# Kernel tuning notes

Measured on AMD Instinct MI355X. Metric: run time of the kernel, lower is better.

The kernel has to match this reference:

```python
import jax, jax.numpy as jnp
import numpy as np

E = 2          # e_layers
DM = 64        # d_model == emb_dim (hardcoded 64 in out_layer)
H = 8          # n_heads
DH = DM // H
DFF = 256      # d_ff
P = 16         # patch_size
STRIDE = P // 2
SL = 4096      # seq_len
NPATCH = (SL - P) // STRIDE + 1   # 511
PRED = 96
B, M = 8, 8
FACTOR = 5
EPS = 1e-5


def setup_inputs() -> dict:
    key = jax.random.key(0)
    ks = jax.random.split(key, 32)
    s = jnp.float32(0.02)
    f = lambda i, shape: jax.random.normal(ks[i], shape, jnp.float32)
    d = {
        "x_enc": f(0, (B, SL, M)),
        "x_mark_enc": f(1, (B, SL, 4)),
        "x_dec": f(2, (B, PRED, M)),
        "x_mark_dec": f(3, (B, PRED, 4)),
        # patch embedding  Linear(patch_size -> emb_dim)
        "in_W": f(4, (DM, P)) * s,
        "in_b": jnp.zeros((DM,), jnp.float32),
        # per-layer attention projections (stacked over e_layers)
        "Wq": f(5, (E, DM, DM)) * s, "bq": jnp.zeros((E, DM), jnp.float32),
        "Wk": f(6, (E, DM, DM)) * s, "bk": jnp.zeros((E, DM), jnp.float32),
        "Wv": f(7, (E, DM, DM)) * s, "bv": jnp.zeros((E, DM), jnp.float32),
        "Wo": f(8, (E, DM, DM)) * s, "bo": jnp.zeros((E, DM), jnp.float32),
        # FFN (Conv1d kernel=1 == Linear)
        "c1_W": f(9, (E, DFF, DM)) * s, "c1_b": jnp.zeros((E, DFF), jnp.float32),
        "c2_W": f(10, (E, DM, DFF)) * s, "c2_b": jnp.zeros((E, DM), jnp.float32),
        # layer norms
        "ln1_g": jnp.ones((E, DM), jnp.float32), "ln1_b": jnp.zeros((E, DM), jnp.float32),
        "ln2_g": jnp.ones((E, DM), jnp.float32), "ln2_b": jnp.zeros((E, DM), jnp.float32),
        "lnf_g": jnp.ones((DM,), jnp.float32), "lnf_b": jnp.zeros((DM,), jnp.float32),
        # decode head  Linear(64*num_patches -> pred_len)
        "out_W": f(11, (PRED, DM * NPATCH)) * s,
        "out_b": jnp.zeros((PRED,), jnp.float32),
    }
    return d


def _ln(x, g, b):
    mu = x.mean(-1, keepdims=True)
    var = ((x - mu) ** 2).mean(-1, keepdims=True)
    return (x - mu) * jax.lax.rsqrt(var + EPS) * g + b


def _prob_attn(q, k, v, key):
    # q,k,v: [Bn, H, L, Dh]  (ProbSparse attention, mask_flag=False)
    Bn, h, Lq, Dh = q.shape
    Lk = k.shape[2]
    U_part = min(int(FACTOR * np.ceil(np.log(Lk))), Lk)   # sampled keys per query
    u = min(int(FACTOR * np.ceil(np.log(Lq))), Lq)        # top-u active queries
    idx = jax.random.randint(key, (Lq, U_part), 0, Lk)
    k_sample = k[:, :, idx, :]                             # [Bn,H,Lq,U,Dh]
    qk_sample = jnp.einsum('bhld,bhlud->bhlu', q, k_sample)
    # sparsity measure: max - sum/L_K (as in torch code)
    sparsity = qk_sample.max(-1) - qk_sample.sum(-1) / jnp.float32(Lk)
    _, top_idx = jax.lax.top_k(sparsity, u)                # [Bn,H,u]
    q_red = jnp.take_along_axis(q, top_idx[..., None], axis=2)  # [Bn,H,u,Dh]
    scale = jax.lax.rsqrt(jnp.float32(Dh))
    scores = jnp.einsum('bhud,bhkd->bhuk', q_red, k) * scale    # [Bn,H,u,Lk]
    attn = jax.nn.softmax(scores, axis=-1)
    # lazy context: mean of V for inactive queries, attn@V for active ones
    ctx = jnp.broadcast_to(v.mean(axis=2, keepdims=True), q.shape)
    upd = jnp.einsum('bhuk,bhkd->bhud', attn, v)
    bi = jnp.arange(Bn)[:, None, None]
    hi = jnp.arange(h)[None, :, None]
    ctx = ctx.at[bi, hi, top_idx].set(upd)
    return ctx.transpose(0, 2, 1, 3)  # [Bn,L,H,Dh]


def reference(x_enc, x_mark_enc, x_dec, x_mark_dec, in_W, in_b, Wq, bq, Wk, bk,
              Wv, bv, Wo, bo, c1_W, c1_b, c2_W, c2_b, ln1_g, ln1_b, ln2_g, ln2_b,
              lnf_g, lnf_b, out_W, out_b):
    Bb, L, Mm = x_enc.shape
    x = x_enc.transpose(0, 2, 1)  # b l m -> b m l
    pidx = jnp.arange(NPATCH)[:, None] * STRIDE + jnp.arange(P)[None, :]
    patches = x[:, :, pidx]                         # [B,M,N,P] (unfold)
    z = patches.reshape(Bb * Mm, NPATCH, P) @ in_W.T + in_b  # [BM,N,DM]
    akey = jax.random.key(1)
    for e in range(E):
        q = (z @ Wq[e].T + bq[e]).reshape(Bb * Mm, NPATCH, H, DH).transpose(0, 2, 1, 3)
        k = (z @ Wk[e].T + bk[e]).reshape(Bb * Mm, NPATCH, H, DH).transpose(0, 2, 1, 3)
        v = (z @ Wv[e].T + bv[e]).reshape(Bb * Mm, NPATCH, H, DH).transpose(0, 2, 1, 3)
        ctx = _prob_attn(q, k, v, jax.random.fold_in(akey, e))
        new_x = ctx.reshape(Bb * Mm, NPATCH, DM) @ Wo[e].T + bo[e]
        x1 = _ln(z + new_x, ln1_g[e], ln1_b[e])
        y = jax.nn.gelu(x1 @ c1_W[e].T + c1_b[e], approximate=False)
        y = y @ c2_W[e].T + c2_b[e]
        z = _ln(x1 + y, ln2_g[e], ln2_b[e])
    z = _ln(z, lnf_g, lnf_b)
    out = z.reshape(Bb * Mm, -1) @ out_W.T + out_b   # [BM, pred_len]
    out = out.reshape(Bb, Mm, PRED).transpose(0, 2, 1)  # (b m) l -> b l m
    return out[:, -PRED:, :]
```

## Files before the change

kernel.cpp:

```cpp
#include <hip/hip_runtime.h>
#include <hip/hip_bf16.h>
#include <stdint.h>
#include <math.h>

typedef __hip_bfloat16 bf16;
typedef __attribute__((ext_vector_type(8))) short short8;
typedef __attribute__((ext_vector_type(4))) short short4v;
typedef __attribute__((ext_vector_type(4))) float fx4;

#define NP 511
#define UPART 35
#define NTOK 32704
#define NBITS 17885
#define LN_EPS 1e-5f

__host__ __device__ __forceinline__ void tf2x32(uint32_t k0, uint32_t k1,
                                                uint32_t x0, uint32_t x1,
                                                uint32_t* o0, uint32_t* o1) {
  uint32_t ks2 = k0 ^ k1 ^ 0x1BD11BDAu;
  x0 += k0; x1 += k1;
#define TFR(r) { x0 += x1; x1 = (x1 << (r)) | (x1 >> (32 - (r))); x1 ^= x0; }
  TFR(13) TFR(15) TFR(26) TFR(6)   x0 += k1;  x1 += ks2 + 1u;
  TFR(17) TFR(29) TFR(16) TFR(24)  x0 += ks2; x1 += k0 + 2u;
  TFR(13) TFR(15) TFR(26) TFR(6)   x0 += k0;  x1 += k1 + 3u;
  TFR(17) TFR(29) TFR(16) TFR(24)  x0 += k1;  x1 += ks2 + 4u;
  TFR(13) TFR(15) TFR(26) TFR(6)   x0 += ks2; x1 += k0 + 5u;
#undef TFR
  *o0 = x0; *o1 = x1;
}

__device__ __forceinline__ float ldin(const void* p, int i, int f32) {
  if (f32) return ((const float*)p)[i];
  return __bfloat162float(((const bf16*)p)[i]);
}
__device__ __forceinline__ unsigned short f2bf(float v) {
  uint32_t u = __builtin_bit_cast(uint32_t, v);
  u += 0x7fffu + ((u >> 16) & 1u);
  return (unsigned short)(u >> 16);
}
__device__ __forceinline__ float bfb2f(uint32_t h) {
  uint32_t u = h << 16;
  return __builtin_bit_cast(float, u);
}
__device__ __forceinline__ float lo16(uint32_t w) { return bfb2f(w & 0xFFFFu); }
__device__ __forceinline__ float hi16(uint32_t w) { return bfb2f(w >> 16); }
__device__ __forceinline__ uint32_t pack2(float a, float b) {
  return (uint32_t)f2bf(a) | ((uint32_t)f2bf(b) << 16);
}
__device__ __forceinline__ int lanes_below(unsigned long long m) {
  return __builtin_amdgcn_mbcnt_hi((uint32_t)(m >> 32),
         __builtin_amdgcn_mbcnt_lo((uint32_t)m, 0));
}

__global__ void probe_kernel(const uint32_t* __restrict__ lnfg,
                             int* __restrict__ flag) {
  if (blockIdx.x == 0 && threadIdx.x == 0)
    flag[0] = (lnfg[0] == 0x3F800000u) ? 1 : 0;
}

__global__ void zero_out_kernel(bf16* __restrict__ out, int n) {
  int i = blockIdx.x * 256 + threadIdx.x;
  if (i < n) out[i] = __float2bfloat16(0.f);
}

__global__ void gen_idx_kernel(int* __restrict__ idxT,
    uint32_t ka0, uint32_t ka1, uint32_t kb0, uint32_t kb1) {
  int i = blockIdx.x * 256 + threadIdx.x;
  if (i >= 2 * NBITS) return;
  int e = i / NBITS;
  uint32_t j = (uint32_t)(i - e * NBITS);
  uint32_t k0 = e ? kb0 : ka0, k1 = e ? kb1 : ka1;
  uint32_t o0, o1;
  tf2x32(k0, k1, 0u, j, &o0, &o1);
  uint32_t bits = o1;
  uint32_t hi = bits >> 16, lo = bits & 0xFFFFu;
  uint32_t off = ((hi % 511u) * 32u + (lo % 511u)) % 511u;
  int l = (int)(j / UPART), u = (int)(j % UPART);
  idxT[e * NBITS + u * NP + l] = (int)off;
}

__global__ __launch_bounds__(256) void embed_kernel(
    const void* __restrict__ xe, const void* __restrict__ inW,
    const void* __restrict__ inb, float* __restrict__ z,
    const int* __restrict__ flg) {
  __shared__ float xs[136 * 8];
  int f = flg[0];
  int b = blockIdx.x >> 5, nt = blockIdx.x & 31;
  int n0 = nt * 16;
  for (int i = threadIdx.x; i < 1088; i += 256) {
    int row = i >> 3, m = i & 7;
    int g = n0 * 8 + row;
    xs[i] = (g < 4096) ? ldin(xe, (b * 4096 + g) * 8 + m, f) : 0.f;
  }
  int d = threadIdx.x & 63, mg = threadIdx.x >> 6;
  float wreg[16];
#pragma unroll
  for (int p = 0; p < 16; ++p) wreg[p] = ldin(inW, d * 16 + p, f);
  float bd = ldin(inb, d, f);
  __syncthreads();
  for (int nl = 0; nl < 16; ++nl) {
    int n = n0 + nl;
    if (n >= NP) break;
#pragma unroll
    for (int mm = 0; mm < 2; ++mm) {
      int m = mg * 2 + mm;
      float acc = bd;
#pragma unroll
      for (int p = 0; p < 16; ++p)
        acc = fmaf(xs[(nl * 8 + p) * 8 + m], wreg[p], acc);
      int t = (b * 8 + m) * NP + n;
      z[(size_t)t * 64 + d] = acc;
    }
  }
}

__global__ __launch_bounds__(256) void qkv_kernel(
    const float* __restrict__ z,
    const void* __restrict__ Wq, const void* __restrict__ bq,
    const void* __restrict__ Wk, const void* __restrict__ bk,
    const void* __restrict__ Wv, const void* __restrict__ bv,
    bf16* __restrict__ qb, bf16* __restrict__ kb, bf16* __restrict__ vb,
    const int* __restrict__ flg, int e) {
  __shared__ short xb[64 * 72];
  __shared__ short wL[192 * 72];
  __shared__ float bqs[192];
  int f = flg[0];
  int t0 = blockIdx.x * 64;
  int tid = threadIdx.x;
  {
    const float4* xg = (const float4*)(z + (size_t)t0 * 64);
#pragma unroll
    for (int r = 0; r < 4; ++r) {
      int i4 = r * 256 + tid;
      float4 v = xg[i4];
      int t = (i4 * 4) >> 6, d = (i4 * 4) & 63;
      short4v h;
      h.x = (short)f2bf(v.x); h.y = (short)f2bf(v.y);
      h.z = (short)f2bf(v.z); h.w = (short)f2bf(v.w);
      *(short4v*)&xb[t * 72 + d] = h;
    }
  }
  if (!f) {
    const uint4* Wg0 = (const uint4*)((const bf16*)Wq + e * 4096);
    const uint4* Wg1 = (const uint4*)((const bf16*)Wk + e * 4096);
    const uint4* Wg2 = (const uint4*)((const bf16*)Wv + e * 4096);
#pragma unroll
    for (int r = 0; r < 2; ++r) {
      int i = r * 256 + tid;
      int row = i >> 3, c8 = (i & 7) * 8;
      *(uint4*)&wL[row * 72 + c8] = Wg0[i];
      *(uint4*)&wL[(64 + row) * 72 + c8] = Wg1[i];
      *(uint4*)&wL[(128 + row) * 72 + c8] = Wg2[i];
    }
  } else {
#pragma unroll
    for (int r = 0; r < 16; ++r) {
      int i = r * 256 + tid;
      int row = i >> 6, c = i & 63;
      wL[row * 72 + c] = (short)f2bf(((const float*)Wq)[e * 4096 + i]);
      wL[(64 + row) * 72 + c] = (short)f2bf(((const float*)Wk)[e * 4096 + i]);
      wL[(128 + row) * 72 + c] = (short)f2bf(((const float*)Wv)[e * 4096 + i]);
    }
  }
  if (tid < 192) {
    int t3 = tid >> 6, j = tid & 63;
    bqs[tid] = (t3 == 0) ? ldin(bq, e * 64 + j, f)
             : (t3 == 1) ? ldin(bk, e * 64 + j, f)
                         : ldin(bv, e * 64 + j, f);
  }
  __syncthreads();
  int lane = tid & 63, w = tid >> 6;
  int m0 = w * 16, col = lane & 15, quad = lane >> 4;
  short8 a0 = *(const short8*)&xb[(m0 + col) * 72 + quad * 8];
  short8 a1 = *(const short8*)&xb[(m0 + col) * 72 + 32 + quad * 8];
#pragma unroll
  for (int nt = 0; nt < 12; ++nt) {
    fx4 acc = {0.f, 0.f, 0.f, 0.f};
    short8 b0 = *(const short8*)&wL[(nt * 16 + col) * 72 + quad * 8];
    short8 b1 = *(const short8*)&wL[(nt * 16 + col) * 72 + 32 + quad * 8];
    acc = __builtin_amdgcn_mfma_f32_16x16x32_bf16(a0, b0, acc, 0, 0, 0);
    acc = __builtin_amdgcn_mfma_f32_16x16x32_bf16(a1, b1, acc, 0, 0, 0);
    int c = nt * 16 + col;
    int t3 = c >> 6, hd = c & 63, h = hd >> 3, d2 = hd & 7;
    bf16* base = (t3 == 0) ? qb : (t3 == 1) ? kb : vb;
    float bia = bqs[c];
#pragma unroll
    for (int reg = 0; reg < 4; ++reg) {
      int tok = t0 + m0 + quad * 4 + reg;
      int bm = tok / NP, n = tok - bm * NP;
      base[((size_t)(bm * 8 + h) * NP + n) * 8 + d2] =
          __float2bfloat16(acc[reg] + bia);
    }
  }
}

__global__ __launch_bounds__(256) void attn_sparse_kernel(
    const bf16* __restrict__ qg, const bf16* __restrict__ kg,
    const int* __restrict__ idxT, float* __restrict__ sparsg) {
  __shared__ uint32_t kkp[NP * 5 + 3];
  __shared__ float mx2[128], sm2[128];
  int blk = blockIdx.x;
  int bh = blk >> 2, q4 = blk & 3;
  int bm = bh >> 3, h = bh & 7;
  size_t hb = (size_t)(bm * 8 + h) * NP * 8;
  {
    const uint4* k4 = (const uint4*)(kg + hb);
    for (int n = threadIdx.x; n < NP; n += 256) {
      uint4 b = k4[n];
      uint32_t* dk = kkp + n * 5;
      dk[0] = b.x; dk[1] = b.y; dk[2] = b.z; dk[3] = b.w;
    }
  }
  __syncthreads();
  int lq = threadIdx.x & 127, half = threadIdx.x >> 7;
  int l = q4 * 128 + lq;
  float mx = -1e30f, sm = 0.f;
  if (l < NP) {
    uint4 a = ((const uint4*)(qg + hb))[l];
    float ql[8];
    ql[0] = lo16(a.x); ql[1] = hi16(a.x);
    ql[2] = lo16(a.y); ql[3] = hi16(a.y);
    ql[4] = lo16(a.z); ql[5] = hi16(a.z);
    ql[6] = lo16(a.w); ql[7] = hi16(a.w);
    int u0 = half ? 18 : 0, u1 = half ? 35 : 18;
#pragma unroll 6
    for (int u = u0; u < u1; ++u) {
      int j = idxT[u * NP + l];
      j = ((unsigned)j > 510u) ? 0 : j;
      const uint32_t* kr = kkp + j * 5;
      uint32_t w0 = kr[0], w1 = kr[1], w2 = kr[2], w3 = kr[3];
      float dt = 0.f;
      dt = fmaf(ql[0], lo16(w0), dt); dt = fmaf(ql[1], hi16(w0), dt);
      dt = fmaf(ql[2], lo16(w1), dt); dt = fmaf(ql[3], hi16(w1), dt);
      dt = fmaf(ql[4], lo16(w2), dt); dt = fmaf(ql[5], hi16(w2), dt);
      dt = fmaf(ql[6], lo16(w3), dt); dt = fmaf(ql[7], hi16(w3), dt);
      mx = fmaxf(mx, dt); sm += dt;
    }
  }
  if (half) { mx2[lq] = mx; sm2[lq] = sm; }
  __syncthreads();
  if (!half && l < NP) {
    float m = fmaxf(mx, mx2[lq]);
    float s = sm + sm2[lq];
    sparsg[(size_t)bh * NP + l] = m - s * (1.0f / 511.0f);
  }
}

__global__ __launch_bounds__(512) void attn_soft_kernel(
    const bf16* __restrict__ qg, const bf16* __restrict__ kg,
    const bf16* __restrict__ vg, const float* __restrict__ sparsg,
    bf16* __restrict__ ctx) {
  __shared__ uint32_t kkp[NP * 5 + 3];
  __shared__ uint32_t kvp[NP * 5 + 3];
  __shared__ float scF[8 * 512];
  __shared__ float redv[256];
  __shared__ int topi[UPART];
  __shared__ float vmean[8];
  __shared__ unsigned char selflag[NP + 1];
  int blk = blockIdx.x;
  int bh = blk >> 1, half = blk & 1;
  int bm = bh >> 3, h = bh & 7;
  size_t hb = (size_t)(bm * 8 + h) * NP * 8;
  int lane = threadIdx.x & 63;
  if (threadIdx.x < 64) {
    const float* sp = sparsg + (size_t)bh * NP;
    uint32_t key[8];
#pragma unroll
    for (int jj = 0; jj < 8; ++jj) {
      int ll = lane + jj * 64;
      if (ll < NP) {
        uint32_t u = __builtin_bit_cast(uint32_t, sp[ll]);
        key[jj] = (u & 0x80000000u) ? ~u : (u | 0x80000000u);
      } else key[jj] = 0u;
    }
    uint32_t p = 0u;
    for (int b = 31; b >= 0; --b) {
      uint32_t t = p | (1u << b);
      int cnt = 0;
#pragma unroll
      for (int jj = 0; jj < 8; ++jj)
        cnt += __popcll(__ballot(key[jj] >= t));
      if (cnt >= UPART) p = t;
    }
    int c1 = 0;
#pragma unroll
    for (int jj = 0; jj < 8; ++jj)
      c1 += __popcll(__ballot(key[jj] > p));
    int need = UPART - c1;
    int base = 0, taken = 0;
#pragma unroll
    for (int jj = 0; jj < 8; ++jj) {
      int ll = lane + jj * 64;
      bool gt = key[jj] > p;
      bool eq = key[jj] == p;
      unsigned long long meq = __ballot(eq);
      int beq = lanes_below(meq);
      bool sel = gt || (eq && (taken + beq) < need);
      unsigned long long msel = __ballot(sel);
      int pos = base + lanes_below(msel);
      if (sel) topi[pos] = ll;
      if (ll < NP) selflag[ll] = sel ? 1 : 0;
      base += __popcll(msel);
      taken += __popcll(meq);
    }
  } else {
    const uint4* k4 = (const uint4*)(kg + hb);
    const uint4* v4 = (const uint4*)(vg + hb);
    for (int n = threadIdx.x - 64; n < NP; n += 448) {
      uint4 b = k4[n], c = v4[n];
      uint32_t* dk = kkp + n * 5;
      uint32_t* dv = kvp + n * 5;
      dk[0] = b.x; dk[1] = b.y; dk[2] = b.z; dk[3] = b.w;
      dv[0] = c.x; dv[1] = c.y; dv[2] = c.z; dv[3] = c.w;
    }
  }
  __syncthreads();
  if (threadIdx.x < 256) {
    int d = threadIdx.x & 7, pt = threadIdx.x >> 3;
    int c = d >> 1, odd = d & 1;
    float s = 0.f;
    for (int n = pt; n < NP; n += 32) {
      uint32_t w = kvp[n * 5 + c];
      s += odd ? hi16(w) : lo16(w);
    }
    redv[threadIdx.x] = s;
  }
  __syncthreads();
  if (threadIdx.x < 8) {
    float s = 0.f;
#pragma unroll
    for (int pt = 0; pt < 32; ++pt) s += redv[pt * 8 + threadIdx.x];
    vmean[threadIdx.x] = s * (1.0f / 511.0f);
  }
  __syncthreads();
  size_t cb = (size_t)bm * (NP * 64) + h * 8;
  if (threadIdx.x < 256) {
    int n = half * 256 + threadIdx.x;
    if (n < NP && !selflag[n]) {
      uint4 pv;
      pv.x = pack2(vmean[0], vmean[1]);
      pv.y = pack2(vmean[2], vmean[3]);
      pv.z = pack2(vmean[4], vmean[5]);
      pv.w = pack2(vmean[6], vmean[7]);
      *(uint4*)(ctx + cb + (size_t)n * 64) = pv;
    }
  }
  int wv = threadIdx.x >> 6;
  const float scale = 0.35355339059327373f;
  float* myS = scF + wv * 512;
  int u0 = half + 2 * wv;
  int l0 = topi[u0];
  int l1 = topi[u0 + 16];
  bool has3 = (u0 + 32) < UPART;
  int l2 = has3 ? topi[u0 + 32] : l0;
  l0 = ((unsigned)l0 > 510u) ? 0 : l0;
  l1 = ((unsigned)l1 > 510u) ? 0 : l1;
  l2 = ((unsigned)l2 > 510u) ? 0 : l2;
  const uint4* q4p = (const uint4*)(qg + hb);
  uint4 qv0 = q4p[l0];
  uint4 qv1 = q4p[l1];
  uint4 qv2 = q4p[l2];

  auto process = [&](uint4 a, int lsel) {
    float qs[8];
    qs[0] = lo16(a.x); qs[1] = hi16(a.x);
    qs[2] = lo16(a.y); qs[3] = hi16(a.y);
    qs[4] = lo16(a.z); qs[5] = hi16(a.z);
    qs[6] = lo16(a.w); qs[7] = hi16(a.w);
    float mx = -1e30f;
    for (int j = lane; j < NP; j += 64) {
      const uint32_t* kr = kkp + j * 5;
      uint32_t w0 = kr[0], w1 = kr[1], w2 = kr[2], w3 = kr[3];
      float d0 = qs[0] * lo16(w0);
      d0 = fmaf(qs[1], hi16(w0), d0);
      d0 = fmaf(qs[2], lo16(w1), d0);
      d0 = fmaf(qs[3], hi16(w1), d0);
      float d1 = qs[4] * lo16(w2);
      d1 = fmaf(qs[5], hi16(w2), d1);
      d1 = fmaf(qs[6], lo16(w3), d1);
      d1 = fmaf(qs[7], hi16(w3), d1);
      float sc = (d0 + d1) * scale;
      myS[j] = sc;
      mx = fmaxf(mx, sc);
    }
    for (int off = 32; off; off >>= 1) mx = fmaxf(mx, __shfl_xor(mx, off));
    float ssum = 0.f, acc[8];
#pragma unroll
    for (int d2 = 0; d2 < 8; ++d2) acc[d2] = 0.f;
    for (int j = lane; j < NP; j += 64) {
      float w = __expf(myS[j] - mx);
      ssum += w;
      const uint32_t* vr = kvp + j * 5;
      uint32_t x0 = vr[0], x1 = vr[1], x2 = vr[2], x3 = vr[3];
      acc[0] = fmaf(w, lo16(x0), acc[0]); acc[1] = fmaf(w, hi16(x0), acc[1]);
      acc[2] = fmaf(w, lo16(x1), acc[2]); acc[3] = fmaf(w, hi16(x1), acc[3]);
      acc[4] = fmaf(w, lo16(x2), acc[4]); acc[5] = fmaf(w, hi16(x2), acc[5]);
      acc[6] = fmaf(w, lo16(x3), acc[6]); acc[7] = fmaf(w, hi16(x3), acc[7]);
    }
    for (int off = 32; off; off >>= 1) {
      ssum += __shfl_xor(ssum, off);
#pragma unroll
      for (int d2 = 0; d2 < 8; ++d2) acc[d2] += __shfl_xor(acc[d2], off);
    }
    if (lane == 0) {
      float inv = 1.0f / ssum;
      uint4 pv;
      pv.x = pack2(acc[0] * inv, acc[1] * inv);
      pv.y = pack2(acc[2] * inv, acc[3] * inv);
      pv.z = pack2(acc[4] * inv, acc[5] * inv);
      pv.w = pack2(acc[6] * inv, acc[7] * inv);
      *(uint4*)(ctx + cb + (size_t)lsel * 64) = pv;
    }
  };
  process(qv0, l0);
  process(qv1, l1);
  if (has3) process(qv2, l2);
}

__global__ __launch_bounds__(256) void oproj_ln_kernel(
    const float* __restrict__ z, const bf16* __restrict__ ctx,
    const void* __restrict__ Wo, const void* __restrict__ bo,
    const void* __restrict__ g, const void* __restrict__ bb,
    float* __restrict__ x1, const int* __restrict__ flg, int e) {
  __shared__ short cbL[64 * 72];
  __shared__ short woL[64 * 72];
  __shared__ float zf[64 * 64];
  __shared__ float bos[64], gs[64], bbs[64];
  int f = flg[0];
  int t0 = blockIdx.x * 64;
  int tid = threadIdx.x;
  {
    const uint4* cg = (const uint4*)(ctx + (size_t)t0 * 64);
#pragma unroll
    for (int r = 0; r < 2; ++r) {
      int i = r * 256 + tid;
      uint4 v = cg[i];
      int row = i >> 3, c8 = (i & 7) * 8;
      *(uint4*)&cbL[row * 72 + c8] = v;
    }
    const float4* zg = (const float4*)(z + (size_t)t0 * 64);
#pragma unroll
    for (int r = 0; r < 4; ++r) {
      int i4 = r * 256 + tid;
      float4 v = zg[i4];
      int t = (i4 * 4) >> 6, d = (i4 * 4) & 63;
      *(float4*)&zf[t * 64 + d] = v;
    }
  }
  if (!f) {
    const uint4* Wg = (const uint4*)((const bf16*)Wo + e * 4096);
#pragma unroll
    for (int r = 0; r < 2; ++r) {
      int i = r * 256 + tid;
      int row = i >> 3, c8 = (i & 7) * 8;
      *(uint4*)&woL[row * 72 + c8] = Wg[i];
    }
  } else {
#pragma unroll
    for (int r = 0; r < 16; ++r) {
      int i = r * 256 + tid;
      int row = i >> 6, c = i & 63;
      woL[row * 72 + c] = (short)f2bf(((const float*)Wo)[e * 4096 + i]);
    }
  }
  if (tid < 64) {
    bos[tid] = ldin(bo, e * 64 + tid, f);
    gs[tid] = ldin(g, e * 64 + tid, f);
    bbs[tid] = ldin(bb, e * 64 + tid, f);
  }
  __syncthreads();
  int lane = tid & 63, w = tid >> 6;
  int m0 = w * 16, col = lane & 15, quad = lane >> 4;
  short8 a0 = *(const short8*)&cbL[(m0 + col) * 72 + quad * 8];
  short8 a1 = *(const short8*)&cbL[(m0 + col) * 72 + 32 + quad * 8];
  fx4 vacc[4];
#pragma unroll
  for (int nt = 0; nt < 4; ++nt) {
    fx4 acc = {0.f, 0.f, 0.f, 0.f};
    short8 b0 = *(const short8*)&woL[(nt * 16 + col) * 72 + quad * 8];
    short8 b1 = *(const short8*)&woL[(nt * 16 + col) * 72 + 32 + quad * 8];
    acc = __builtin_amdgcn_mfma_f32_16x16x32_bf16(a0, b0, acc, 0, 0, 0);
    acc = __builtin_amdgcn_mfma_f32_16x16x32_bf16(a1, b1, acc, 0, 0, 0);
    vacc[nt] = acc;
  }
  float vals[4][4];
  float ps[4], sq[4];
#pragma unroll
  for (int reg = 0; reg < 4; ++reg) { ps[reg] = 0.f; sq[reg] = 0.f; }
#pragma unroll
  for (int nt = 0; nt < 4; ++nt) {
    int d = nt * 16 + col;
#pragma unroll
    for (int reg = 0; reg < 4; ++reg) {
      int tl = m0 + quad * 4 + reg;
      float v = vacc[nt][reg] + bos[d] + zf[tl * 64 + d];
      vals[nt][reg] = v;
      ps[reg] += v; sq[reg] += v * v;
    }
  }
#pragma unroll
  for (int off = 1; off < 16; off <<= 1) {
#pragma unroll
    for (int reg = 0; reg < 4; ++reg) {
      ps[reg] += __shfl_xor(ps[reg], off);
      sq[reg] += __shfl_xor(sq[reg], off);
    }
  }
#pragma unroll
  for (int reg = 0; reg < 4; ++reg) {
    float mu = ps[reg] * (1.0f / 64.0f);
    float var = sq[reg] * (1.0f / 64.0f) - mu * mu;
    float rs = rsqrtf(fmaxf(var, 0.f) + LN_EPS);
    int tl = m0 + quad * 4 + reg;
#pragma unroll
    for (int nt = 0; nt < 4; ++nt) {
      int d = nt * 16 + col;
      x1[(size_t)(t0 + tl) * 64 + d] = (vals[nt][reg] - mu) * rs * gs[d] + bbs[d];
    }
  }
}

__global__ __launch_bounds__(256) void ffn_kernel(
    const float* __restrict__ x1,
    const void* __restrict__ W1, const void* __restrict__ b1,
    const void* __restrict__ W2, const void* __restrict__ b2,
    const void* __restrict__ g, const void* __restrict__ bb,
    float* __restrict__ zo, bf16* __restrict__ zfT,
    const void* __restrict__ lfg, const void* __restrict__ lfb,
    const int* __restrict__ flg, int e, int last) {
  __shared__ __align__(16) char smem[72960];
  short* wA  = (short*)smem;
  short* rB  = (short*)(smem + 36864);
  float* b1s = (float*)(smem + 70656);
  float* b2s = b1s + 256;
  float* gs  = b2s + 64;
  float* bbs = gs + 64;
  float* g2s = bbs + 64;
  float* bb2s = g2s + 64;
  int f = flg[0];
  int t0 = blockIdx.x * 64;
  int tid = threadIdx.x;
  {
    const float4* xg = (const float4*)(x1 + (size_t)t0 * 64);
#pragma unroll
    for (int r = 0; r < 4; ++r) {
      int i4 = r * 256 + tid;
      float4 v = xg[i4];
      int t = (i4 * 4) >> 6, d = (i4 * 4) & 63;
      short4v h;
      h.x = (short)f2bf(v.x); h.y = (short)f2bf(v.y);
      h.z = (short)f2bf(v.z); h.w = (short)f2bf(v.w);
      *(short4v*)&rB[t * 72 + d] = h;
    }
  }
  if (!f) {
    const uint4* W1g = (const uint4*)((const bf16*)W1 + e * 16384);
#pragma unroll
    for (int r = 0; r < 8; ++r) {
      int i = r * 256 + tid;
      uint4 v = W1g[i];
      int j = i >> 3, k = (i & 7) * 8;
      *(uint4*)&wA[j * 72 + k] = v;
    }
  } else {
    for (int r = 0; r < 64; ++r) {
      int i = r * 256 + tid;
      int j = i >> 6, k = i & 63;
      wA[j * 72 + k] = (short)f2bf(((const float*)W1)[e * 16384 + i]);
    }
  }
  b1s[tid] = ldin(b1, e * 256 + tid, f);
  if (tid < 64) {
    b2s[tid] = ldin(b2, e * 64 + tid, f);
    gs[tid] = ldin(g, e * 64 + tid, f);
    bbs[tid] = ldin(bb, e * 64 + tid, f);
    g2s[tid] = ldin(lfg, tid, f);
    bb2s[tid] = ldin(lfb, tid, f);
  }
  __syncthreads();

  int lane = tid & 63, w = tid >> 6;
  int m0 = w * 16;
  int col = lane & 15, quad = lane >> 4;
  short8 a0 = *(const short8*)&rB[(m0 + col) * 72 + quad * 8];
  short8 a1 = *(const short8*)&rB[(m0 + col) * 72 + 32 + quad * 8];
  __syncthreads();
#pragma unroll 4
  for (int nt = 0; nt < 16; ++nt) {
    fx4 acc = {0.f, 0.f, 0.f, 0.f};
    short8 bf0 = *(const short8*)&wA[(nt * 16 + col) * 72 + quad * 8];
    short8 bf1 = *(const short8*)&wA[(nt * 16 + col) * 72 + 32 + quad * 8];
    acc = __builtin_amdgcn_mfma_f32_16x16x32_bf16(a0, bf0, acc, 0, 0, 0);
    acc = __builtin_amdgcn_mfma_f32_16x16x32_bf16(a1, bf1, acc, 0, 0, 0);
    int j = nt * 16 + col;
    float bj = b1s[j];
#pragma unroll
    for (int reg = 0; reg < 4; ++reg) {
      float a = acc[reg] + bj;
      float ge = 0.5f * a * (1.0f + erff(a * 0.70710678118654752f));
      rB[(m0 + quad * 4 + reg) * 264 + j] = (short)f2bf(ge);
    }
  }
  __syncthreads();
  if (!f) {
    const uint4* W2g = (const uint4*)((const bf16*)W2 + e * 16384);
#pragma unroll
    for (int r = 0; r < 8; ++r) {
      int i = r * 256 + tid;
      uint4 v2 = W2g[i];
      int dd = i >> 5, c = (i & 31) * 8;
      *(uint4*)&wA[dd * 264 + c] = v2;
    }
  } else {
    for (int r = 0; r < 64; ++r) {
      int i = r * 256 + tid;
      int dd = i >> 8, c = i & 255;
      wA[dd * 264 + c] = (short)f2bf(((const float*)W2)[e * 16384 + i]);
    }
  }
  __syncthreads();
  short8 af[8];
#pragma unroll
  for (int kt = 0; kt < 8; ++kt)
    af[kt] = *(const short8*)&rB[(m0 + col) * 264 + kt * 32 + quad * 8];
  fx4 vacc[4];
#pragma unroll
  for (int nt = 0; nt < 4; ++nt) {
    fx4 acc = {0.f, 0.f, 0.f, 0.f};
#pragma unroll
    for (int kt = 0; kt < 8; ++kt) {
      short8 bfr = *(const short8*)&wA[(nt * 16 + col) * 264 + kt * 32 + quad * 8];
      acc = __builtin_amdgcn_mfma_f32_16x16x32_bf16(af[kt], bfr, acc, 0, 0, 0);
    }
    vacc[nt] = acc;
  }
  float vals[4][4];
  float ps[4], sq[4];
#pragma unroll
  for (int reg = 0; reg < 4; ++reg) { ps[reg] = 0.f; sq[reg] = 0.f; }
#pragma unroll
  for (int nt = 0; nt < 4; ++nt) {
    int d = nt * 16 + col;
#pragma unroll
    for (int reg = 0; reg < 4; ++reg) {
      int tl = m0 + quad * 4 + reg;
      float v = vacc[nt][reg] + b2s[d] + x1[(size_t)(t0 + tl) * 64 + d];
      vals[nt][reg] = v;
      ps[reg] += v; sq[reg] += v * v;
    }
  }
#pragma unroll
  for (int off = 1; off < 16; off <<= 1) {
#pragma unroll
    for (int reg = 0; reg < 4; ++reg) {
      ps[reg] += __shfl_xor(ps[reg], off);
      sq[reg] += __shfl_xor(sq[reg], off);
    }
  }
  if (!last) {
#pragma unroll
    for (int reg = 0; reg < 4; ++reg) {
      float mu = ps[reg] * (1.0f / 64.0f);
      float var = sq[reg] * (1.0f / 64.0f) - mu * mu;
      float rs = rsqrtf(fmaxf(var, 0.f) + LN_EPS);
      int tl = m0 + quad * 4 + reg;
#pragma unroll
      for (int nt = 0; nt < 4; ++nt) {
        int d = nt * 16 + col;
        zo[(size_t)(t0 + tl) * 64 + d] = (vals[nt][reg] - mu) * rs * gs[d] + bbs[d];
      }
    }
  } else {
    float ps2[4], sq2[4];
#pragma unroll
    for (int reg = 0; reg < 4; ++reg) { ps2[reg] = 0.f; sq2[reg] = 0.f; }
    float v2s[4][4];
#pragma unroll
    for (int reg = 0; reg < 4; ++reg) {
      float mu = ps[reg] * (1.0f / 64.0f);
      float var = sq[reg] * (1.0f / 64.0f) - mu * mu;
      float rs = rsqrtf(fmaxf(var, 0.f) + LN_EPS);
#pragma unroll
      for (int nt = 0; nt < 4; ++nt) {
        int d = nt * 16 + col;
        float v2 = (vals[nt][reg] - mu) * rs * gs[d] + bbs[d];
        v2s[nt][reg] = v2;
        ps2[reg] += v2; sq2[reg] += v2 * v2;
      }
    }
#pragma unroll
    for (int off = 1; off < 16; off <<= 1) {
#pragma unroll
      for (int reg = 0; reg < 4; ++reg) {
        ps2[reg] += __shfl_xor(ps2[reg], off);
        sq2[reg] += __shfl_xor(sq2[reg], off);
      }
    }
#pragma unroll
    for (int reg = 0; reg < 4; ++reg) {
      float mu = ps2[reg] * (1.0f / 64.0f);
      float var = sq2[reg] * (1.0f / 64.0f) - mu * mu;
      float rs = rsqrtf(fmaxf(var, 0.f) + LN_EPS);
      int tok = t0 + m0 + quad * 4 + reg;
      int bm = tok / NP, n = tok - bm * NP;
#pragma unroll
      for (int nt = 0; nt < 4; ++nt) {
        int d = nt * 16 + col;
        zfT[(size_t)n * 4096 + bm * 64 + d] =
            __float2bfloat16((v2s[nt][reg] - mu) * rs * g2s[d] + bb2s[d]);
      }
    }
  }
}

__global__ __launch_bounds__(256) void head1_kernel(
    const bf16* __restrict__ zfT, const void* __restrict__ W,
    float* __restrict__ partial, const int* __restrict__ flg) {
  __shared__ short aL[64 * 72];
  __shared__ short bL[96 * 72];
  int f = flg[0];
  int n = blockIdx.x;
  int tid = threadIdx.x;
  {
    const uint4* Ag = (const uint4*)(zfT + (size_t)n * 4096);
#pragma unroll
    for (int r = 0; r < 2; ++r) {
      int i = r * 256 + tid;
      uint4 v = Ag[i];
      int row = i >> 3, c = (i & 7) * 8;
      *(uint4*)&aL[row * 72 + c] = v;
    }
  }
  if (!f) {
    const uint4* Wg = (const uint4*)W;
#pragma unroll
    for (int r = 0; r < 3; ++r) {
      int i = r * 256 + tid;
      int p = i >> 3, c8 = i & 7;
      uint4 v = Wg[(size_t)p * 4088 + n * 8 + c8];
      *(uint4*)&bL[p * 72 + c8 * 8] = v;
    }
  } else {
    for (int r = 0; r < 24; ++r) {
      int i = r * 256 + tid;
      int p = i >> 6, c = i & 63;
      bL[p * 72 + c] = (short)f2bf(((const float*)W)[(size_t)p * 32704 + n * 64 + c]);
    }
  }
  __syncthreads();
  int lane = tid & 63, w = tid >> 6;
  int m0 = w * 16, col = lane & 15, quad = lane >> 4;
  short8 a0 = *(const short8*)&aL[(m0 + col) * 72 + quad * 8];
  short8 a1 = *(const short8*)&aL[(m0 + col) * 72 + 32 + quad * 8];
  float* pb = partial + (size_t)n * 6144;
#pragma unroll
  for (int nt = 0; nt < 6; ++nt) {
    fx4 acc = {0.f, 0.f, 0.f, 0.f};
    short8 b0 = *(const short8*)&bL[(nt * 16 + col) * 72 + quad * 8];
    short8 b1 = *(const short8*)&bL[(nt * 16 + col) * 72 + 32 + quad * 8];
    acc = __builtin_amdgcn_mfma_f32_16x16x32_bf16(a0, b0, acc, 0, 0, 0);
    acc = __builtin_amdgcn_mfma_f32_16x16x32_bf16(a1, b1, acc, 0, 0, 0);
#pragma unroll
    for (int reg = 0; reg < 4; ++reg)
      pb[(m0 + quad * 4 + reg) * 96 + nt * 16 + col] = acc[reg];
  }
}

__global__ __launch_bounds__(256) void head2_kernel(
    const float* __restrict__ partial, const void* __restrict__ bias,
    void* __restrict__ out, const int* __restrict__ flg) {
  __shared__ float red[4][64];
  int f = flg[0];
  int lane = threadIdx.x & 63, w = threadIdx.x >> 6;
  int j = blockIdx.x * 64 + lane;
  float acc = 0.f;
  for (int n = w; n < NP; n += 4)
    acc += partial[(size_t)n * 6144 + j];
  red[w][lane] = acc;
  __syncthreads();
  if (w == 0) {
    float s = red[0][lane] + red[1][lane] + red[2][lane] + red[3][lane];
    int bm = j / 96, p = j - bm * 96;
    float val = s + ldin(bias, p, f);
    int b = bm >> 3, m = bm & 7;
    int o = (b * 96 + p) * 8 + m;
    if (f) ((float*)out)[o] = val;
    else   ((bf16*)out)[o] = __float2bfloat16(val);
  }
}

extern "C" void kernel_launch(void* const* d_in, const int* in_sizes, int n_in,
                              void* d_out, int out_size, void* d_ws, size_t ws_size,
                              hipStream_t stream) {
  const void* xe  = d_in[0];
  const void* inW = d_in[4];
  const void* inb = d_in[5];
  const void* Wq  = d_in[6];
  const void* bq  = d_in[7];
  const void* Wk  = d_in[8];
  const void* bk  = d_in[9];
  const void* Wv  = d_in[10];
  const void* bv  = d_in[11];
  const void* Wo  = d_in[12];
  const void* bo  = d_in[13];
  const void* c1W = d_in[14];
  const void* c1b = d_in[15];
  const void* c2W = d_in[16];
  const void* c2b = d_in[17];
  const void* l1g = d_in[18];
  const void* l1b = d_in[19];
  const void* l2g = d_in[20];
  const void* l2b = d_in[21];
  const void* lfg = d_in[22];
  const void* lfb = d_in[23];
  const void* oW  = d_in[24];
  const void* obv = d_in[25];

  const size_t NF = (size_t)NTOK * 64;
  const size_t SPARS = (size_t)512 * NP;
  const size_t REQ = (3 * NF + 2 * NBITS + 32 + SPARS) * sizeof(float);
  if (ws_size < REQ) {
    zero_out_kernel<<<(out_size + 255) / 256, 256, 0, stream>>>((bf16*)d_out, out_size);
    return;
  }

  float* z   = (float*)d_ws;
  bf16* ctxb = (bf16*)(z + NF);
  bf16* qb   = (bf16*)(z + NF + NF / 2);
  bf16* kb   = (bf16*)(z + 2 * NF);
  bf16* vb   = (bf16*)(z + 2 * NF + NF / 2);
  float* x1  = z + 2 * NF;
  int* idxb  = (int*)(z + 3 * NF);
  int* flg   = idxb + 2 * NBITS;
  float* sparsg = (float*)(flg + 16);
  bf16* zfT  = ctxb;
  float* partial = z;

  probe_kernel<<<1, 64, 0, stream>>>((const uint32_t*)lfg, flg);

  uint32_t ke[2][2];
  for (int e = 0; e < 2; ++e)
    tf2x32(0u, 1u, 0u, (uint32_t)e, &ke[e][0], &ke[e][1]);
  gen_idx_kernel<<<(2 * NBITS + 255) / 256, 256, 0, stream>>>(idxb,
      ke[0][0], ke[0][1], ke[1][0], ke[1][1]);

  embed_kernel<<<256, 256, 0, stream>>>(xe, inW, inb, z, flg);
  for (int e = 0; e < 2; ++e) {
    qkv_kernel<<<NTOK / 64, 256, 0, stream>>>(z, Wq, bq, Wk, bk, Wv, bv,
        qb, kb, vb, flg, e);
    attn_sparse_kernel<<<2048, 256, 0, stream>>>(qb, kb, idxb + e * NBITS,
        sparsg);
    attn_soft_kernel<<<1024, 512, 0, stream>>>(qb, kb, vb, sparsg, ctxb);
    oproj_ln_kernel<<<NTOK / 64, 256, 0, stream>>>(z, ctxb, Wo, bo, l1g, l1b,
        x1, flg, e);
    ffn_kernel<<<NTOK / 64, 256, 0, stream>>>(x1, c1W, c1b, c2W, c2b,
        l2g, l2b, z, zfT, lfg, lfb, flg, e, e == 1);
  }
  head1_kernel<<<NP, 256, 0, stream>>>(zfT, oW, partial, flg);
  head2_kernel<<<96, 256, 0, stream>>>(partial, obv, d_out, flg);
}
```

Baseline: 331.5 us.

## Fuse sparsity-measure and softmax attention kernels into one per-head block

Merges the sparse query-measure kernel and the top-u softmax kernel into one kernel, with one 512-thread block per (batch, head). The sparsity scores now stay in shared memory instead of going through global memory, and K is staged into LDS once instead of twice. The probe kernel is also folded into gen_idx to save a launch. The cost is far fewer blocks (512 instead of 1024/2048), so there is less parallelism and each wave handles up to five selected queries instead of three.

Result: faster. 317.7 us (-4.2%).

```diff
diff --git a/kernel.cpp b/kernel.cpp
--- a/kernel.cpp
+++ b/kernel.cpp
@@ -52,19 +52,16 @@
          __builtin_amdgcn_mbcnt_lo((uint32_t)m, 0));
 }
 
-__global__ void probe_kernel(const uint32_t* __restrict__ lnfg,
-                             int* __restrict__ flag) {
-  if (blockIdx.x == 0 && threadIdx.x == 0)
-    flag[0] = (lnfg[0] == 0x3F800000u) ? 1 : 0;
-}
-
 __global__ void zero_out_kernel(bf16* __restrict__ out, int n) {
   int i = blockIdx.x * 256 + threadIdx.x;
   if (i < n) out[i] = __float2bfloat16(0.f);
 }
 
 __global__ void gen_idx_kernel(int* __restrict__ idxT,
-    uint32_t ka0, uint32_t ka1, uint32_t kb0, uint32_t kb1) {
+    uint32_t ka0, uint32_t ka1, uint32_t kb0, uint32_t kb1,
+    const uint32_t* __restrict__ lnfg, int* __restrict__ flag) {
+  if (blockIdx.x == 0 && threadIdx.x == 0)
+    flag[0] = (lnfg[0] == 0x3F800000u) ? 1 : 0;
   int i = blockIdx.x * 256 + threadIdx.x;
   if (i >= 2 * NBITS) return;
   int e = i / NBITS;
@@ -194,37 +191,46 @@
   }
 }
 
-__global__ __launch_bounds__(256) void attn_sparse_kernel(
+__global__ __launch_bounds__(512) void attn_fused_kernel(
     const bf16* __restrict__ qg, const bf16* __restrict__ kg,
-    const int* __restrict__ idxT, float* __restrict__ sparsg) {
+    const bf16* __restrict__ vg, const int* __restrict__ idxT,
+    bf16* __restrict__ ctx) {
   __shared__ uint32_t kkp[NP * 5 + 3];
-  __shared__ float mx2[128], sm2[128];
-  int blk = blockIdx.x;
-  int bh = blk >> 2, q4 = blk & 3;
+  __shared__ uint32_t kvp[NP * 5 + 3];
+  __shared__ float scF[8 * 512];
+  __shared__ float spars[512];
+  __shared__ float redv[256];
+  __shared__ int topi[UPART];
+  __shared__ float vmean[8];
+  __shared__ unsigned char selflag[NP + 1];
+  int bh = blockIdx.x;
   int bm = bh >> 3, h = bh & 7;
-  size_t hb = (size_t)(bm * 8 + h) * NP * 8;
+  size_t hb = (size_t)bh * NP * 8;
+  int tid = threadIdx.x;
+  int lane = tid & 63, wv = tid >> 6;
   {
     const uint4* k4 = (const uint4*)(kg + hb);
-    for (int n = threadIdx.x; n < NP; n += 256) {
-      uint4 b = k4[n];
+    const uint4* v4 = (const uint4*)(vg + hb);
+    for (int n = tid; n < NP; n += 512) {
+      uint4 b = k4[n], c = v4[n];
       uint32_t* dk = kkp + n * 5;
+      uint32_t* dv = kvp + n * 5;
       dk[0] = b.x; dk[1] = b.y; dk[2] = b.z; dk[3] = b.w;
-    }
-  }
-  __syncthreads();
-  int lq = threadIdx.x & 127, half = threadIdx.x >> 7;
-  int l = q4 * 128 + lq;
-  float mx = -1e30f, sm = 0.f;
-  if (l < NP) {
+      dv[0] = c.x; dv[1] = c.y; dv[2] = c.z; dv[3] = c.w;
+    }
+  }
+  __syncthreads();
+  if (tid < NP) {
+    int l = tid;
     uint4 a = ((const uint4*)(qg + hb))[l];
     float ql[8];
     ql[0] = lo16(a.x); ql[1] = hi16(a.x);
     ql[2] = lo16(a.y); ql[3] = hi16(a.y);
     ql[4] = lo16(a.z); ql[5] = hi16(a.z);
     ql[6] = lo16(a.w); ql[7] = hi16(a.w);
-    int u0 = half ? 18 : 0, u1 = half ? 35 : 18;
+    float mxA = -1e30f, smA = 0.f, mxB = -1e30f, smB = 0.f;
 #pragma unroll 6
-    for (int u = u0; u < u1; ++u) {
+    for (int u = 0; u < 18; ++u) {
       int j = idxT[u * NP + l];
       j = ((unsigned)j > 510u) ? 0 : j;
       const uint32_t* kr = kkp + j * 5;
@@ -234,42 +240,31 @@
       dt = fmaf(ql[2], lo16(w1), dt); dt = fmaf(ql[3], hi16(w1), dt);
       dt = fmaf(ql[4], lo16(w2), dt); dt = fmaf(ql[5], hi16(w2), dt);
       dt = fmaf(ql[6], lo16(w3), dt); dt = fmaf(ql[7], hi16(w3), dt);
-      mx = fmaxf(mx, dt); sm += dt;
-    }
-  }
-  if (half) { mx2[lq] = mx; sm2[lq] = sm; }
-  __syncthreads();
-  if (!half && l < NP) {
-    float m = fmaxf(mx, mx2[lq]);
-    float s = sm + sm2[lq];
-    sparsg[(size_t)bh * NP + l] = m - s * (1.0f / 511.0f);
-  }
-}
-
-__global__ __launch_bounds__(512) void attn_soft_kernel(
-    const bf16* __restrict__ qg, const bf16* __restrict__ kg,
-    const bf16* __restrict__ vg, const float* __restrict__ sparsg,
-    bf16* __restrict__ ctx) {
-  __shared__ uint32_t kkp[NP * 5 + 3];
-  __shared__ uint32_t kvp[NP * 5 + 3];
-  __shared__ float scF[8 * 512];
-  __shared__ float redv[256];
-  __shared__ int topi[UPART];
-  __shared__ float vmean[8];
-  __shared__ unsigned char selflag[NP + 1];
-  int blk = blockIdx.x;
-  int bh = blk >> 1, half = blk & 1;
-  int bm = bh >> 3, h = bh & 7;
-  size_t hb = (size_t)(bm * 8 + h) * NP * 8;
-  int lane = threadIdx.x & 63;
-  if (threadIdx.x < 64) {
-    const float* sp = sparsg + (size_t)bh * NP;
+      mxA = fmaxf(mxA, dt); smA += dt;
+    }
+#pragma unroll 6
+    for (int u = 18; u < 35; ++u) {
+      int j = idxT[u * NP + l];
+      j = ((unsigned)j > 510u) ? 0 : j;
+      const uint32_t* kr = kkp + j * 5;
+      uint32_t w0 = kr[0], w1 = kr[1], w2 = kr[2], w3 = kr[3];
+      float dt = 0.f;
+      dt = fmaf(ql[0], lo16(w0), dt); dt = fmaf(ql[1], hi16(w0), dt);
+      dt = fmaf(ql[2], lo16(w1), dt); dt = fmaf(ql[3], hi16(w1), dt);
+      dt = fmaf(ql[4], lo16(w2), dt); dt = fmaf(ql[5], hi16(w2), dt);
+      dt = fmaf(ql[6], lo16(w3), dt); dt = fmaf(ql[7], hi16(w3), dt);
+      mxB = fmaxf(mxB, dt); smB += dt;
+    }
+    spars[l] = fmaxf(mxA, mxB) - (smA + smB) * (1.0f / 511.0f);
+  }
+  __syncthreads();
+  if (tid < 64) {
     uint32_t key[8];
 #pragma unroll
     for (int jj = 0; jj < 8; ++jj) {
       int ll = lane + jj * 64;
       if (ll < NP) {
-        uint32_t u = __builtin_bit_cast(uint32_t, sp[ll]);
+        uint32_t u = __builtin_bit_cast(uint32_t, spars[ll]);
         key[jj] = (u & 0x80000000u) ? ~u : (u | 0x80000000u);
       } else key[jj] = 0u;
     }
@@ -303,63 +298,53 @@
       base += __popcll(msel);
       taken += __popcll(meq);
     }
-  } else {
-    const uint4* k4 = (const uint4*)(kg + hb);
-    const uint4* v4 = (const uint4*)(vg + hb);
-    for (int n = threadIdx.x - 64; n < NP; n += 448) {
-      uint4 b = k4[n], c = v4[n];
-      uint32_t* dk = kkp + n * 5;
-      uint32_t* dv = kvp + n * 5;
-      dk[0] = b.x; dk[1] = b.y; dk[2] = b.z; dk[3] = b.w;
-      dv[0] = c.x; dv[1] = c.y; dv[2] = c.z; dv[3] = c.w;
-    }
-  }
-  __syncthreads();
-  if (threadIdx.x < 256) {
-    int d = threadIdx.x & 7, pt = threadIdx.x >> 3;
+  } else if (tid >= 256) {
+    int tt = tid - 256;
+    int d = tt & 7, pt = tt >> 3;
     int c = d >> 1, odd = d & 1;
     float s = 0.f;
     for (int n = pt; n < NP; n += 32) {
       uint32_t w = kvp[n * 5 + c];
       s += odd ? hi16(w) : lo16(w);
     }
-    redv[threadIdx.x] = s;
-  }
-  __syncthreads();
-  if (threadIdx.x < 8) {
+    redv[tt] = s;
+  }
+  __syncthreads();
+  if (tid < 8) {
     float s = 0.f;
 #pragma unroll
-    for (int pt = 0; pt < 32; ++pt) s += redv[pt * 8 + threadIdx.x];
-    vmean[threadIdx.x] = s * (1.0f / 511.0f);
+    for (int pt = 0; pt < 32; ++pt) s += redv[pt * 8 + tid];
+    vmean[tid] = s * (1.0f / 511.0f);
   }
   __syncthreads();
   size_t cb = (size_t)bm * (NP * 64) + h * 8;
-  if (threadIdx.x < 256) {
-    int n = half * 256 + threadIdx.x;
-    if (n < NP && !selflag[n]) {
-      uint4 pv;
-      pv.x = pack2(vmean[0], vmean[1]);
-      pv.y = pack2(vmean[2], vmean[3]);
-      pv.z = pack2(vmean[4], vmean[5]);
-      pv.w = pack2(vmean[6], vmean[7]);
-      *(uint4*)(ctx + cb + (size_t)n * 64) = pv;
-    }
-  }
-  int wv = threadIdx.x >> 6;
+  if (tid < NP && !selflag[tid]) {
+    uint4 pv;
+    pv.x = pack2(vmean[0], vmean[1]);
+    pv.y = pack2(vmean[2], vmean[3]);
+    pv.z = pack2(vmean[4], vmean[5]);
+    pv.w = pack2(vmean[6], vmean[7]);
+    *(uint4*)(ctx + cb + (size_t)tid * 64) = pv;
+  }
   const float scale = 0.35355339059327373f;
   float* myS = scF + wv * 512;
-  int u0 = half + 2 * wv;
-  int l0 = topi[u0];
-  int l1 = topi[u0 + 16];
-  bool has3 = (u0 + 32) < UPART;
-  int l2 = has3 ? topi[u0 + 32] : l0;
+  int l0 = topi[wv];
+  int l1 = topi[wv + 8];
+  int l2 = topi[wv + 16];
+  int l3 = topi[wv + 24];
+  bool has5 = (wv + 32) < UPART;
+  int l4 = has5 ? topi[wv + 32] : l0;
   l0 = ((unsigned)l0 > 510u) ? 0 : l0;
   l1 = ((unsigned)l1 > 510u) ? 0 : l1;
   l2 = ((unsigned)l2 > 510u) ? 0 : l2;
+  l3 = ((unsigned)l3 > 510u) ? 0 : l3;
+  l4 = ((unsigned)l4 > 510u) ? 0 : l4;
   const uint4* q4p = (const uint4*)(qg + hb);
   uint4 qv0 = q4p[l0];
   uint4 qv1 = q4p[l1];
   uint4 qv2 = q4p[l2];
+  uint4 qv3 = q4p[l3];
+  uint4 qv4 = q4p[l4];
 
   auto process = [&](uint4 a, int lsel) {
     float qs[8];
@@ -414,7 +399,9 @@
   };
   process(qv0, l0);
   process(qv1, l1);
-  if (has3) process(qv2, l2);
+  process(qv2, l2);
+  process(qv3, l3);
+  if (has5) process(qv4, l4);
 }
 
 __global__ __launch_bounds__(256) void oproj_ln_kernel(
@@ -817,8 +804,7 @@
   const void* obv = d_in[25];
 
   const size_t NF = (size_t)NTOK * 64;
-  const size_t SPARS = (size_t)512 * NP;
-  const size_t REQ = (3 * NF + 2 * NBITS + 32 + SPARS) * sizeof(float);
+  const size_t REQ = (3 * NF + 2 * NBITS + 32) * sizeof(float);
   if (ws_size < REQ) {
     zero_out_kernel<<<(out_size + 255) / 256, 256, 0, stream>>>((bf16*)d_out, out_size);
     return;
@@ -832,25 +818,21 @@
   float* x1  = z + 2 * NF;
   int* idxb  = (int*)(z + 3 * NF);
   int* flg   = idxb + 2 * NBITS;
-  float* sparsg = (float*)(flg + 16);
   bf16* zfT  = ctxb;
   float* partial = z;
-
-  probe_kernel<<<1, 64, 0, stream>>>((const uint32_t*)lfg, flg);
 
   uint32_t ke[2][2];
   for (int e = 0; e < 2; ++e)
     tf2x32(0u, 1u, 0u, (uint32_t)e, &ke[e][0], &ke[e][1]);
   gen_idx_kernel<<<(2 * NBITS + 255) / 256, 256, 0, stream>>>(idxb,
-      ke[0][0], ke[0][1], ke[1][0], ke[1][1]);
+      ke[0][0], ke[0][1], ke[1][0], ke[1][1], (const uint32_t*)lfg, flg);
 
   embed_kernel<<<256, 256, 0, stream>>>(xe, inW, inb, z, flg);
   for (int e = 0; e < 2; ++e) {
     qkv_kernel<<<NTOK / 64, 256, 0, stream>>>(z, Wq, bq, Wk, bk, Wv, bv,
         qb, kb, vb, flg, e);
-    attn_sparse_kernel<<<2048, 256, 0, stream>>>(qb, kb, idxb + e * NBITS,
-        sparsg);
-    attn_soft_kernel<<<1024, 512, 0, stream>>>(qb, kb, vb, sparsg, ctxb);
+    attn_fused_kernel<<<512, 512, 0, stream>>>(qb, kb, vb, idxb + e * NBITS,
+        ctxb);
     oproj_ln_kernel<<<NTOK / 64, 256, 0, stream>>>(z, ctxb, Wo, bo, l1g, l1b,
         x1, flg, e);
     ffn_kernel<<<NTOK / 64, 256, 0, stream>>>(x1, c1W, c1b, c2W, c2b,
```
